# Optimization experiments

Hardware: AMD Instinct MI355X
Metric: run time of the kernel (lower is better)

Reference implementation:

```python
import jax, jax.numpy as jnp
import numpy as np

DIM = 64
HEADS = 8
P = 4  # polarizations
EPS = 1e-12


def _conv2d(x, w, b, groups):
    # x: [N,C,H,W], w: [O, C//groups, kh, kw] (torch OIHW), stride 1, SAME padding
    y = jax.lax.conv_general_dilated(
        x, w, window_strides=(1, 1), padding='SAME',
        dimension_numbers=('NCHW', 'OIHW', 'NCHW'), feature_group_count=groups)
    return y + b[None, :, None, None]


def setup_inputs() -> dict:
    key = jax.random.key(0)
    ks = jax.random.split(key, 12)
    B, C, H, W = 4, DIM, 128, 128
    s = 1.0 / np.sqrt(C)
    x_in = jax.random.normal(ks[0], (B * P, C, H, W), dtype=jnp.float32)
    mask = jax.random.uniform(ks[1], (B * P, C, H, W), dtype=jnp.float32)
    wq = jax.random.normal(ks[2], (C, C), dtype=jnp.float32) * s
    wk = jax.random.normal(ks[3], (C, C), dtype=jnp.float32) * s
    wv = jax.random.normal(ks[4], (C, C), dtype=jnp.float32) * s
    w_proj = jax.random.normal(ks[5], (C, C), dtype=jnp.float32) * s
    b_proj = jax.random.normal(ks[6], (C,), dtype=jnp.float32) * 0.01
    rescale = jnp.ones((HEADS, 1, 1), dtype=jnp.float32)
    dw_w = jax.random.normal(ks[7], (C, 1, 3, 3), dtype=jnp.float32) * (1.0 / 3.0)
    dw_b = jax.random.normal(ks[8], (C,), dtype=jnp.float32) * 0.01
    pw_w = jax.random.normal(ks[9], (C, C, 1, 1), dtype=jnp.float32) * s
    pw_b = jax.random.normal(ks[10], (C,), dtype=jnp.float32) * 0.01
    return {'x_in': x_in, 'mask': mask, 'wq': wq, 'wk': wk, 'wv': wv,
            'w_proj': w_proj, 'b_proj': b_proj, 'rescale': rescale,
            'dw_w': dw_w, 'dw_b': dw_b, 'pw_w': pw_w, 'pw_b': pw_b}


def reference(x_in, mask, wq, wk, wv, w_proj, b_proj, rescale, dw_w, dw_b, pw_w, pw_b):
    bp, c, h, w = x_in.shape
    b_num = bp // P
    dh = c // HEADS
    # 'b p c h w -> (b h w) p c'
    x = x_in.reshape(b_num, P, c, h, w).transpose(0, 3, 4, 1, 2).reshape(b_num * h * w, P, c)
    # torch Linear (no bias): x @ W.T
    q = jnp.einsum('bpc,dc->bpd', x, wq)
    k = jnp.einsum('bpc,dc->bpd', x, wk)
    v = jnp.einsum('bpc,dc->bpd', x, wv)
    # 'b p (h c) -> b h p c'
    q = q.reshape(-1, P, HEADS, dh).transpose(0, 2, 1, 3)
    k = k.reshape(-1, P, HEADS, dh).transpose(0, 2, 1, 3)
    v = v.reshape(-1, P, HEADS, dh).transpose(0, 2, 1, 3)
    # L2 normalize along head dim (torch F.normalize: clamp_min(eps))
    q = q / jnp.maximum(jnp.linalg.norm(q, axis=-1, keepdims=True), EPS)
    k = k / jnp.maximum(jnp.linalg.norm(k, axis=-1, keepdims=True), EPS)
    atten = jnp.einsum('bhpc,bhqc->bhpq', q, k) * rescale  # rescale: [heads,1,1]
    # mask branch: depthwise 3x3 -> GELU(exact) -> pointwise 1x1
    mg = _conv2d(mask, dw_w, dw_b, groups=c)
    mg = jax.nn.gelu(mg, approximate=False)
    mg = _conv2d(mg, pw_w, pw_b, groups=1)
    mg = mg.reshape(b_num, P, c, h, w).mean(axis=2)  # [b,p,h,w]
    mb = mg.transpose(0, 2, 3, 1).reshape(b_num * h * w, P)  # '(b h w) p'
    mask_bias = mb[:, None, :] - mb[:, :, None]  # [B, p, p]
    atten = atten + mask_bias[:, None, :, :]
    atten = jax.nn.softmax(atten, axis=-1)
    out = jnp.einsum('bhpq,bhqc->bhpc', atten, v)
    out = out.transpose(0, 2, 1, 3).reshape(-1, P, c)  # 'b h p c -> b p (h c)'
    out = jnp.einsum('bpc,dc->bpd', out, w_proj) + b_proj
    # '(b h w) p c -> b p c h w' -> [(b p), c, h, w]
    out = out.reshape(b_num, h, w, P, c).transpose(0, 3, 4, 1, 2)
    return out.reshape(b_num * P, c, h, w)
```

## Files before the change

### kernel.cpp

```cpp
#include <hip/hip_runtime.h>

#define HSZ 128
#define WSZ 128
#define HWSZ (HSZ*WSZ)
#define NB 4

#define OFF_CM 0
#define OFF_MB 128

typedef unsigned short u16;
typedef __attribute__((ext_vector_type(8))) short bf16x8;
typedef __attribute__((ext_vector_type(4))) float f32x4;

__device__ __forceinline__ float bf2f(u16 u) {
    return __uint_as_float(((unsigned int)u) << 16);
}
__device__ __forceinline__ u16 f2bf_bits(float f) {
    unsigned int x = __float_as_uint(f);
    return (u16)((x + 0x7fffu + ((x >> 16) & 1u)) >> 16);
}
__device__ __forceinline__ bf16x8 pack8(const float* s) {
    bf16x8 r;
    #pragma unroll
    for (int j = 0; j < 8; ++j) r[j] = (short)f2bf_bits(s[j]);
    return r;
}
__device__ __forceinline__ bf16x8 load_bfrag(const float* W, int drow, int k0) {
    float4 a = *(const float4*)(W + drow*64 + k0);
    float4 b = *(const float4*)(W + drow*64 + k0 + 4);
    float t[8] = {a.x,a.y,a.z,a.w,b.x,b.y,b.z,b.w};
    return pack8(t);
}

__global__ void prep_kernel(const float* __restrict__ pww,
                            float* __restrict__ ws) {
    int t = threadIdx.x;
    if (t < 64) {
        float s = 0.f;
        for (int co = 0; co < 64; ++co) s += pww[co*64 + t];
        ws[OFF_CM + t] = s * (1.0f/64.0f);
    }
}

__global__ __launch_bounds__(1024) void mask_kernel(const float* __restrict__ mask,
                                                    const float* __restrict__ dww,
                                                    const float* __restrict__ dwb,
                                                    float* __restrict__ ws) {
    __shared__ float red[4][256][4];
    int bid = blockIdx.x;
    int bp = bid >> 4;
    int hg = bid & 15;
    int tid = threadIdx.x;
    int cq = tid >> 8;
    int t = tid & 255;
    int h = hg*8 + (t >> 5);
    int w0 = (t & 31) << 2;
    const float* mb_ = mask + (size_t)bp*64*HWSZ;
    int hm = h > 0 ? h-1 : 0;
    int hp = h < 127 ? h+1 : 127;
    float vt = h > 0 ? 1.f : 0.f;
    float vb = h < 127 ? 1.f : 0.f;
    float vl = w0 > 0 ? 1.f : 0.f;
    float vr = w0 < 124 ? 1.f : 0.f;
    int wl = w0 > 0 ? w0-1 : 0;
    int wr = w0 < 124 ? w0+4 : 127;
    const float* cm = ws + OFF_CM;
    float acc0=0.f, acc1=0.f, acc2=0.f, acc3=0.f;
    for (int ci = 0; ci < 16; ++ci) {
        int c = cq*16 + ci;
        const float* rc = mb_ + c*HWSZ;
        const float* r0 = rc + hm*WSZ;
        const float* r1 = rc + h*WSZ;
        const float* r2 = rc + hp*WSZ;
        float4 m0 = *(const float4*)(r0 + w0);
        float4 m1 = *(const float4*)(r1 + w0);
        float4 m2 = *(const float4*)(r2 + w0);
        float L0 = r0[wl]*vl, L1 = r1[wl]*vl, L2 = r2[wl]*vl;
        float R0 = r0[wr]*vr, R1 = r1[wr]*vr, R2 = r2[wr]*vr;
        float w00 = dww[c*9+0]*vt, w01 = dww[c*9+1]*vt, w02 = dww[c*9+2]*vt;
        float w10 = dww[c*9+3],    w11 = dww[c*9+4],    w12 = dww[c*9+5];
        float w20 = dww[c*9+6]*vb, w21 = dww[c*9+7]*vb, w22 = dww[c*9+8]*vb;
        float bb = dwb[c];
        float s0 = bb + w00*L0   + w01*m0.x + w02*m0.y
                      + w10*L1   + w11*m1.x + w12*m1.y
                      + w20*L2   + w21*m2.x + w22*m2.y;
        float s1 = bb + w00*m0.x + w01*m0.y + w02*m0.z
                      + w10*m1.x + w11*m1.y + w12*m1.z
                      + w20*m2.x + w21*m2.y + w22*m2.z;
        float s2 = bb + w00*m0.y + w01*m0.z + w02*m0.w
                      + w10*m1.y + w11*m1.z + w12*m1.w
                      + w20*m2.y + w21*m2.z + w22*m2.w;
        float s3 = bb + w00*m0.z + w01*m0.w + w02*R0
                      + w10*m1.z + w11*m1.w + w12*R1
                      + w20*m2.z + w21*m2.w + w22*R2;
        float cmc = cm[c];
        acc0 += cmc * (0.5f*s0*(1.f + erff(s0*0.70710678118654752f)));
        acc1 += cmc * (0.5f*s1*(1.f + erff(s1*0.70710678118654752f)));
        acc2 += cmc * (0.5f*s2*(1.f + erff(s2*0.70710678118654752f)));
        acc3 += cmc * (0.5f*s3*(1.f + erff(s3*0.70710678118654752f)));
    }
    red[cq][t][0] = acc0;
    red[cq][t][1] = acc1;
    red[cq][t][2] = acc2;
    red[cq][t][3] = acc3;
    __syncthreads();
    if (tid < 256) {
        int b = bp >> 2, p = bp & 3;
        size_t base = (size_t)b*HWSZ + h*WSZ + w0;
        #pragma unroll
        for (int e = 0; e < 4; ++e) {
            float v = red[0][tid][e] + red[1][tid][e] + red[2][tid][e] + red[3][tid][e];
            ws[OFF_MB + (base+e)*4 + p] = v;
        }
    }
}

__global__ __launch_bounds__(256) void attn_kernel(const float* __restrict__ x_in,
                                                   const float* __restrict__ wq,
                                                   const float* __restrict__ wk,
                                                   const float* __restrict__ wv,
                                                   const float* __restrict__ wp,
                                                   const float* __restrict__ bpj,
                                                   const float* __restrict__ rsc,
                                                   const float* __restrict__ ws,
                                                   float* __restrict__ out) {
    __shared__ u16 smem[32768];
    u16* ldsA = smem;
    u16* ldsQ = smem + 8192;
    u16* ldsK = smem + 16384;
    u16* ldsV = smem + 24576;
    float* outS = (float*)(smem + 8192);

    int t = threadIdx.x;
    int lane = t & 63;
    int wid = __builtin_amdgcn_readfirstlane(t >> 6);
    int n15 = lane & 15;
    int quad = lane >> 4;
    int b = blockIdx.x >> 9;
    int hw0 = (blockIdx.x & 511) << 5;

    bf16x8 fq0 = load_bfrag(wq, wid*16 + n15, quad*8);
    bf16x8 fq1 = load_bfrag(wq, wid*16 + n15, 32 + quad*8);
    bf16x8 fk0 = load_bfrag(wk, wid*16 + n15, quad*8);
    bf16x8 fk1 = load_bfrag(wk, wid*16 + n15, 32 + quad*8);
    bf16x8 fv0 = load_bfrag(wv, wid*16 + n15, quad*8);
    bf16x8 fv1 = load_bfrag(wv, wid*16 + n15, 32 + quad*8);
    bf16x8 fp0 = load_bfrag(wp, wid*16 + n15, quad*8);
    bf16x8 fp1 = load_bfrag(wp, wid*16 + n15, 32 + quad*8);
    float bias = bpj[wid*16 + n15];

    for (int it = 0; it < 8; ++it) {
        int i = t + (it << 8);
        int row = i >> 3;
        int l4 = i & 7;
        float4 xv = *(const float4*)(x_in + (size_t)(b*256 + row)*HWSZ + hw0 + l4*4);
        int p = row >> 6, c = row & 63;
        int kt = c >> 5, qd = (c >> 3) & 3, j = c & 7;
        float vals[4] = {xv.x, xv.y, xv.z, xv.w};
        #pragma unroll
        for (int e = 0; e < 4; ++e) {
            int tau = (p << 5) + (l4 << 2) + e;
            int slot = (tau & 15) | (qd << 4);
            ldsA[((tau >> 4)*2 + kt)*512 + slot*8 + j] = f2bf_bits(vals[e]);
        }
    }
    __syncthreads();

    for (int mt = 0; mt < 8; ++mt) {
        bf16x8 a0 = *(const bf16x8*)(ldsA + mt*1024 + lane*8);
        bf16x8 a1 = *(const bf16x8*)(ldsA + mt*1024 + 512 + lane*8);
        f32x4 aq = {0.f,0.f,0.f,0.f};
        f32x4 ak = {0.f,0.f,0.f,0.f};
        f32x4 av = {0.f,0.f,0.f,0.f};
        aq = __builtin_amdgcn_mfma_f32_16x16x32_bf16(a0, fq0, aq, 0, 0, 0);
        aq = __builtin_amdgcn_mfma_f32_16x16x32_bf16(a1, fq1, aq, 0, 0, 0);
        ak = __builtin_amdgcn_mfma_f32_16x16x32_bf16(a0, fk0, ak, 0, 0, 0);
        ak = __builtin_amdgcn_mfma_f32_16x16x32_bf16(a1, fk1, ak, 0, 0, 0);
        av = __builtin_amdgcn_mfma_f32_16x16x32_bf16(a0, fv0, av, 0, 0, 0);
        av = __builtin_amdgcn_mfma_f32_16x16x32_bf16(a1, fv1, av, 0, 0, 0);
        int cb = (mt*4 + wid)*256 + n15;
        #pragma unroll
        for (int r = 0; r < 4; ++r) {
            int rl = (quad*4 + r)*16;
            ldsQ[cb + rl] = f2bf_bits(aq[r]);
            ldsK[cb + rl] = f2bf_bits(ak[r]);
            ldsV[cb + rl] = f2bf_bits(av[r]);
        }
    }
    __syncthreads();

    {
        int pix = t & 31;
        int hd = t >> 5;
        float qv[4][8], kv[4][8], vv[4][8];
        #pragma unroll
        for (int p = 0; p < 4; ++p) {
            int tau = (p << 5) + pix;
            int base = ((tau >> 4)*4 + (hd >> 1))*256 + (tau & 15)*16 + (hd & 1)*8;
            bf16x8 q8 = *(const bf16x8*)(ldsQ + base);
            bf16x8 k8 = *(const bf16x8*)(ldsK + base);
            bf16x8 v8 = *(const bf16x8*)(ldsV + base);
            #pragma unroll
            for (int j = 0; j < 8; ++j) {
                qv[p][j] = bf2f((u16)q8[j]);
                kv[p][j] = bf2f((u16)k8[j]);
                vv[p][j] = bf2f((u16)v8[j]);
            }
        }
        #pragma unroll
        for (int p = 0; p < 4; ++p) {
            float sq = 0.f, sk = 0.f;
            #pragma unroll
            for (int j = 0; j < 8; ++j) { sq += qv[p][j]*qv[p][j]; sk += kv[p][j]*kv[p][j]; }
            float iq = 1.0f / fmaxf(sqrtf(sq), 1e-12f);
            float ik = 1.0f / fmaxf(sqrtf(sk), 1e-12f);
            #pragma unroll
            for (int j = 0; j < 8; ++j) { qv[p][j] *= iq; kv[p][j] *= ik; }
        }
        float4 mb4 = *(const float4*)(ws + OFF_MB + ((size_t)b*HWSZ + hw0 + pix)*4);
        float mba[4] = {mb4.x, mb4.y, mb4.z, mb4.w};
        float rs = rsc[hd];
        float at[4][4];
        #pragma unroll
        for (int p = 0; p < 4; ++p) {
            #pragma unroll
            for (int r = 0; r < 4; ++r) {
                float d = 0.f;
                #pragma unroll
                for (int j = 0; j < 8; ++j) d += qv[p][j]*kv[r][j];
                at[p][r] = d*rs + mba[r];
            }
            float m = fmaxf(fmaxf(at[p][0], at[p][1]), fmaxf(at[p][2], at[p][3]));
            float e0 = expf(at[p][0]-m), e1 = expf(at[p][1]-m);
            float e2 = expf(at[p][2]-m), e3 = expf(at[p][3]-m);
            float inv = 1.0f / (e0+e1+e2+e3);
            at[p][0]=e0*inv; at[p][1]=e1*inv; at[p][2]=e2*inv; at[p][3]=e3*inv;
        }
        #pragma unroll
        for (int p = 0; p < 4; ++p) {
            float y[8];
            #pragma unroll
            for (int j = 0; j < 8; ++j) {
                y[j] = at[p][0]*vv[0][j] + at[p][1]*vv[1][j]
                     + at[p][2]*vv[2][j] + at[p][3]*vv[3][j];
            }
            int tau = (p << 5) + pix;
            int idx = ((tau >> 4)*2 + (hd >> 2))*512 + ((tau & 15) + ((hd & 3) << 4))*8;
            *(bf16x8*)(ldsA + idx) = pack8(y);
        }
    }
    __syncthreads();

    for (int mt = 0; mt < 8; ++mt) {
        bf16x8 a0 = *(const bf16x8*)(ldsA + mt*1024 + lane*8);
        bf16x8 a1 = *(const bf16x8*)(ldsA + mt*1024 + 512 + lane*8);
        f32x4 ao = {0.f,0.f,0.f,0.f};
        ao = __builtin_amdgcn_mfma_f32_16x16x32_bf16(a0, fp0, ao, 0, 0, 0);
        ao = __builtin_amdgcn_mfma_f32_16x16x32_bf16(a1, fp1, ao, 0, 0, 0);
        #pragma unroll
        for (int r = 0; r < 4; ++r) {
            int tau = mt*16 + quad*4 + r;
            int d = wid*16 + n15;
            outS[tau*64 + (d ^ (tau & 31))] = ao[r] + bias;
        }
    }
    __syncthreads();
    for (int g = 0; g < 32; ++g) {
        int flat = (g << 8) + t;
        int px = flat & 31;
        int pd = flat >> 5;
        int d = pd & 63;
        int p = pd >> 6;
        int tau = (p << 5) + px;
        out[(size_t)((b*4 + p)*64 + d)*HWSZ + hw0 + px] = outS[tau*64 + (d ^ (tau & 31))];
    }
}

extern "C" void kernel_launch(void* const* d_in, const int* in_sizes, int n_in,
                              void* d_out, int out_size, void* d_ws, size_t ws_size,
                              hipStream_t stream) {
    const float* x_in  = (const float*)d_in[0];
    const float* mask  = (const float*)d_in[1];
    const float* wq    = (const float*)d_in[2];
    const float* wk    = (const float*)d_in[3];
    const float* wv    = (const float*)d_in[4];
    const float* wproj = (const float*)d_in[5];
    const float* bproj = (const float*)d_in[6];
    const float* resc  = (const float*)d_in[7];
    const float* dww   = (const float*)d_in[8];
    const float* dwb   = (const float*)d_in[9];
    const float* pww   = (const float*)d_in[10];
    float* ws = (float*)d_ws;
    float* outp = (float*)d_out;

    hipLaunchKernelGGL(prep_kernel, dim3(1), dim3(64), 0, stream, pww, ws);
    hipLaunchKernelGGL(mask_kernel, dim3(256), dim3(1024), 0, stream,
                       mask, dww, dwb, ws);
    hipLaunchKernelGGL(attn_kernel, dim3(2048), dim3(256), 0, stream,
                       x_in, wq, wk, wv, wproj, bproj, resc, ws, outp);
}
```

Before: 240.2 us.

## Fuse prep into mask kernel, swizzle LDS layouts, use packed bf16 conversion

Removes the separate prep launch by having every mask block recompute the column means of the pointwise weights into shared memory. In the attention kernel the x staging loads two channels at once and writes packed bf16 pairs. The A-tile and Q/K/V LDS layouts are XOR/rotation swizzled to reduce bank conflicts. Scalar bf16 packing is replaced with the hardware packed conversion intrinsic. The cost is a redundant 64x64 reduction in every mask block.

```diff
diff --git a/kernel.cpp b/kernel.cpp
--- a/kernel.cpp
+++ b/kernel.cpp
@@ -1,12 +1,12 @@
 #include <hip/hip_runtime.h>
+#include <hip/hip_bf16.h>
 
 #define HSZ 128
 #define WSZ 128
 #define HWSZ (HSZ*WSZ)
 #define NB 4
 
-#define OFF_CM 0
-#define OFF_MB 128
+#define OFF_MB 0
 
 typedef unsigned short u16;
 typedef __attribute__((ext_vector_type(8))) short bf16x8;
@@ -15,42 +15,44 @@
 __device__ __forceinline__ float bf2f(u16 u) {
     return __uint_as_float(((unsigned int)u) << 16);
 }
+__device__ __forceinline__ unsigned int cvt_pk_bf16(float lo, float hi) {
+    __hip_bfloat162 h = __float22bfloat162_rn(make_float2(lo, hi));
+    return *(unsigned int*)&h;
+}
 __device__ __forceinline__ u16 f2bf_bits(float f) {
     unsigned int x = __float_as_uint(f);
     return (u16)((x + 0x7fffu + ((x >> 16) & 1u)) >> 16);
 }
-__device__ __forceinline__ bf16x8 pack8(const float* s) {
-    bf16x8 r;
-    #pragma unroll
-    for (int j = 0; j < 8; ++j) r[j] = (short)f2bf_bits(s[j]);
-    return r;
+__device__ __forceinline__ int sswz(int s) { return s ^ (s >> 3); }
+__device__ __forceinline__ int qkv_idx(int t, int d) {
+    return (t >> 2)*64 + ((((t & 3) + (t >> 2)) & 3) << 4) + d;
 }
 __device__ __forceinline__ bf16x8 load_bfrag(const float* W, int drow, int k0) {
     float4 a = *(const float4*)(W + drow*64 + k0);
     float4 b = *(const float4*)(W + drow*64 + k0 + 4);
-    float t[8] = {a.x,a.y,a.z,a.w,b.x,b.y,b.z,b.w};
-    return pack8(t);
-}
-
-__global__ void prep_kernel(const float* __restrict__ pww,
-                            float* __restrict__ ws) {
-    int t = threadIdx.x;
-    if (t < 64) {
-        float s = 0.f;
-        for (int co = 0; co < 64; ++co) s += pww[co*64 + t];
-        ws[OFF_CM + t] = s * (1.0f/64.0f);
-    }
+    unsigned int u[4];
+    u[0] = cvt_pk_bf16(a.x, a.y); u[1] = cvt_pk_bf16(a.z, a.w);
+    u[2] = cvt_pk_bf16(b.x, b.y); u[3] = cvt_pk_bf16(b.z, b.w);
+    return *(bf16x8*)u;
 }
 
 __global__ __launch_bounds__(1024) void mask_kernel(const float* __restrict__ mask,
                                                     const float* __restrict__ dww,
                                                     const float* __restrict__ dwb,
+                                                    const float* __restrict__ pww,
                                                     float* __restrict__ ws) {
     __shared__ float red[4][256][4];
+    __shared__ float cmS[64];
+    int tid = threadIdx.x;
+    if (tid < 64) {
+        float s = 0.f;
+        for (int co = 0; co < 64; ++co) s += pww[co*64 + tid];
+        cmS[tid] = s * (1.0f/64.0f);
+    }
+    __syncthreads();
     int bid = blockIdx.x;
     int bp = bid >> 4;
     int hg = bid & 15;
-    int tid = threadIdx.x;
     int cq = tid >> 8;
     int t = tid & 255;
     int h = hg*8 + (t >> 5);
@@ -64,7 +66,6 @@
     float vr = w0 < 124 ? 1.f : 0.f;
     int wl = w0 > 0 ? w0-1 : 0;
     int wr = w0 < 124 ? w0+4 : 127;
-    const float* cm = ws + OFF_CM;
     float acc0=0.f, acc1=0.f, acc2=0.f, acc3=0.f;
     for (int ci = 0; ci < 16; ++ci) {
         int c = cq*16 + ci;
@@ -93,7 +94,7 @@
         float s3 = bb + w00*m0.z + w01*m0.w + w02*R0
                       + w10*m1.z + w11*m1.w + w12*R1
                       + w20*m2.z + w21*m2.w + w22*R2;
-        float cmc = cm[c];
+        float cmc = cmS[c];
         acc0 += cmc * (0.5f*s0*(1.f + erff(s0*0.70710678118654752f)));
         acc1 += cmc * (0.5f*s1*(1.f + erff(s1*0.70710678118654752f)));
         acc2 += cmc * (0.5f*s2*(1.f + erff(s2*0.70710678118654752f)));
@@ -149,26 +150,31 @@
     bf16x8 fp1 = load_bfrag(wp, wid*16 + n15, 32 + quad*8);
     float bias = bpj[wid*16 + n15];
 
-    for (int it = 0; it < 8; ++it) {
+    unsigned int* ldsA32 = (unsigned int*)ldsA;
+    for (int it = 0; it < 4; ++it) {
         int i = t + (it << 8);
-        int row = i >> 3;
-        int l4 = i & 7;
-        float4 xv = *(const float4*)(x_in + (size_t)(b*256 + row)*HWSZ + hw0 + l4*4);
-        int p = row >> 6, c = row & 63;
-        int kt = c >> 5, qd = (c >> 3) & 3, j = c & 7;
-        float vals[4] = {xv.x, xv.y, xv.z, xv.w};
+        int rp = i >> 3, l4 = i & 7;
+        int p = rp >> 5, cp = rp & 31;
+        int c0 = cp*2;
+        const float* r0 = x_in + (size_t)(b*256 + p*64 + c0)*HWSZ + hw0 + l4*4;
+        float4 v0 = *(const float4*)r0;
+        float4 v1 = *(const float4*)(r0 + HWSZ);
+        int kt = c0 >> 5, qd = (c0 >> 3) & 3, j2 = (c0 & 7) >> 1;
+        float a0[4] = {v0.x, v0.y, v0.z, v0.w};
+        float a1[4] = {v1.x, v1.y, v1.z, v1.w};
         #pragma unroll
         for (int e = 0; e < 4; ++e) {
             int tau = (p << 5) + (l4 << 2) + e;
             int slot = (tau & 15) | (qd << 4);
-            ldsA[((tau >> 4)*2 + kt)*512 + slot*8 + j] = f2bf_bits(vals[e]);
-        }
-    }
-    __syncthreads();
-
+            ldsA32[((tau >> 4)*2 + kt)*256 + sswz(slot)*4 + j2] = cvt_pk_bf16(a0[e], a1[e]);
+        }
+    }
+    __syncthreads();
+
+    int sl8 = sswz(lane)*8;
     for (int mt = 0; mt < 8; ++mt) {
-        bf16x8 a0 = *(const bf16x8*)(ldsA + mt*1024 + lane*8);
-        bf16x8 a1 = *(const bf16x8*)(ldsA + mt*1024 + 512 + lane*8);
+        bf16x8 a0 = *(const bf16x8*)(ldsA + mt*1024 + sl8);
+        bf16x8 a1 = *(const bf16x8*)(ldsA + mt*1024 + 512 + sl8);
         f32x4 aq = {0.f,0.f,0.f,0.f};
         f32x4 ak = {0.f,0.f,0.f,0.f};
         f32x4 av = {0.f,0.f,0.f,0.f};
@@ -178,13 +184,13 @@
         ak = __builtin_amdgcn_mfma_f32_16x16x32_bf16(a1, fk1, ak, 0, 0, 0);
         av = __builtin_amdgcn_mfma_f32_16x16x32_bf16(a0, fv0, av, 0, 0, 0);
         av = __builtin_amdgcn_mfma_f32_16x16x32_bf16(a1, fv1, av, 0, 0, 0);
-        int cb = (mt*4 + wid)*256 + n15;
+        int tb = (mt*4 + wid)*256;
         #pragma unroll
         for (int r = 0; r < 4; ++r) {
-            int rl = (quad*4 + r)*16;
-            ldsQ[cb + rl] = f2bf_bits(aq[r]);
-            ldsK[cb + rl] = f2bf_bits(ak[r]);
-            ldsV[cb + rl] = f2bf_bits(av[r]);
+            int idx = tb + quad*64 + ((((r + quad) & 3)) << 4) + n15;
+            ldsQ[idx] = f2bf_bits(aq[r]);
+            ldsK[idx] = f2bf_bits(ak[r]);
+            ldsV[idx] = f2bf_bits(av[r]);
         }
     }
     __syncthreads();
@@ -196,7 +202,7 @@
         #pragma unroll
         for (int p = 0; p < 4; ++p) {
             int tau = (p << 5) + pix;
-            int base = ((tau >> 4)*4 + (hd >> 1))*256 + (tau & 15)*16 + (hd & 1)*8;
+            int base = ((tau >> 4)*4 + (hd >> 1))*256 + qkv_idx(tau & 15, (hd & 1)*8);
             bf16x8 q8 = *(const bf16x8*)(ldsQ + base);
             bf16x8 k8 = *(const bf16x8*)(ldsK + base);
             bf16x8 v8 = *(const bf16x8*)(ldsV + base);
@@ -236,6 +242,7 @@
             float inv = 1.0f / (e0+e1+e2+e3);
             at[p][0]=e0*inv; at[p][1]=e1*inv; at[p][2]=e2*inv; at[p][3]=e3*inv;
         }
+        unsigned int* ldsA32w = (unsigned int*)ldsA;
         #pragma unroll
         for (int p = 0; p < 4; ++p) {
             float y[8];
@@ -245,15 +252,18 @@
                      + at[p][2]*vv[2][j] + at[p][3]*vv[3][j];
             }
             int tau = (p << 5) + pix;
-            int idx = ((tau >> 4)*2 + (hd >> 2))*512 + ((tau & 15) + ((hd & 3) << 4))*8;
-            *(bf16x8*)(ldsA + idx) = pack8(y);
+            int slot = (tau & 15) | ((hd & 3) << 4);
+            unsigned int pk[4];
+            pk[0] = cvt_pk_bf16(y[0], y[1]); pk[1] = cvt_pk_bf16(y[2], y[3]);
+            pk[2] = cvt_pk_bf16(y[4], y[5]); pk[3] = cvt_pk_bf16(y[6], y[7]);
+            *(uint4*)(ldsA32w + ((tau >> 4)*2 + (hd >> 2))*256 + sswz(slot)*4) = *(uint4*)pk;
         }
     }
     __syncthreads();
 
     for (int mt = 0; mt < 8; ++mt) {
-        bf16x8 a0 = *(const bf16x8*)(ldsA + mt*1024 + lane*8);
-        bf16x8 a1 = *(const bf16x8*)(ldsA + mt*1024 + 512 + lane*8);
+        bf16x8 a0 = *(const bf16x8*)(ldsA + mt*1024 + sl8);
+        bf16x8 a1 = *(const bf16x8*)(ldsA + mt*1024 + 512 + sl8);
         f32x4 ao = {0.f,0.f,0.f,0.f};
         ao = __builtin_amdgcn_mfma_f32_16x16x32_bf16(a0, fp0, ao, 0, 0, 0);
         ao = __builtin_amdgcn_mfma_f32_16x16x32_bf16(a1, fp1, ao, 0, 0, 0);
@@ -293,9 +303,8 @@
     float* ws = (float*)d_ws;
     float* outp = (float*)d_out;
 
-    hipLaunchKernelGGL(prep_kernel, dim3(1), dim3(64), 0, stream, pww, ws);
     hipLaunchKernelGGL(mask_kernel, dim3(256), dim3(1024), 0, stream,
-                       mask, dww, dwb, ws);
+                       mask, dww, dwb, pww, ws);
     hipLaunchKernelGGL(attn_kernel, dim3(2048), dim3(256), 0, stream,
                        x_in, wq, wk, wv, wproj, bproj, resc, ws, outp);
 }
```

Result: faster. 234.7 us (-2.3%).
